# Kernel optimization log

Hardware: AMD Instinct MI355X
Metric: run time of the kernel (lower is better)

The kernel has to match this reference:

```python
import jax, jax.numpy as jnp
import numpy as np

N = 1024      # number of nodes
D = 128       # d_x
H = 8         # num_heads


def setup_inputs() -> dict:
    key = jax.random.key(0)
    ks = jax.random.split(key, 7)
    s = (D * H) ** -0.5
    return {
        "x": jax.random.normal(ks[0], (N, D), dtype=jnp.float32),
        "spatial_encoding": jax.random.normal(ks[1], (N, N), dtype=jnp.float32),
        "edge_encoding": jax.random.normal(ks[2], (N, N), dtype=jnp.float32),
        "Wq": jax.random.normal(ks[3], (D * H, D), dtype=jnp.float32) * s,
        "Wk": jax.random.normal(ks[4], (D * H, D), dtype=jnp.float32) * s,
        "Wv": jax.random.normal(ks[5], (D * H, D), dtype=jnp.float32) * s,
        "Wo": jax.random.normal(ks[6], (D, D * H), dtype=jnp.float32) * s,
    }


def reference(x, spatial_encoding, edge_encoding, Wq, Wk, Wv, Wo):
    n, d = x.shape
    h = Wq.shape[0] // d
    scale = d ** -0.5
    # Linear (no bias), then the module's peculiar view: [n, d*h] -> [d, n, h]
    q = (x @ Wq.T).reshape(d, n, h)            # [d, n, h]
    k = (x @ Wk.T).reshape(d, n, h)            # [d, n, h]
    v = (x @ Wv.T).reshape(d, n, h)            # [d, n, h]
    # a = q @ k^T over head dim: [d, n, n]
    a = jnp.einsum('dnh,dmh->dnm', q, k) * scale
    a = a + spatial_encoding + edge_encoding   # [n,n] biases broadcast over d
    a = jax.nn.softmax(a, axis=2)
    # dropout is identity at inference
    out = jnp.einsum('dnm,dmh->dnh', a, v)     # [d, n, h]
    out = out.reshape(n, h * d)                # row-major reshape, same as torch
    return out @ Wo.T                          # [n, d]
```

## Files before the change

### kernel.cpp

```cpp
#include <hip/hip_runtime.h>
#include <hip/hip_bf16.h>
#include <math.h>

#define N_NODES 1024
#define D_DIM   128
#define H_HEADS 8
#define DH      1024

typedef short  short8 __attribute__((ext_vector_type(8)));
typedef float  f32x16 __attribute__((ext_vector_type(16)));
typedef float  f32x4  __attribute__((ext_vector_type(4)));

static __device__ __forceinline__ unsigned short f2bf(float x) {
    __hip_bfloat16 h = __float2bfloat16(x);
    return *reinterpret_cast<unsigned short*>(&h);
}
static __device__ __forceinline__ unsigned cvt_pk_bf16(float lo, float hi) {
    unsigned r;
    asm volatile("v_cvt_pk_bf16_f32 %0, %1, %2" : "=v"(r) : "v"(lo), "v"(hi));
    return r;
}
static __device__ __forceinline__ void permlane32_swap(unsigned &a, unsigned &b) {
    asm volatile("v_permlane32_swap_b32 %0, %1" : "+v"(a), "+v"(b));
}
static __device__ __forceinline__ float fast_exp2(float x) {
    float r;
    asm("v_exp_f32 %0, %1" : "=v"(r) : "v"(x));
    return r;
}

__global__ __launch_bounds__(256) void prep_kernel(const float* __restrict__ x,
                                                   const float* __restrict__ Wq,
                                                   const float* __restrict__ Wk,
                                                   const float* __restrict__ Wv,
                                                   const float* __restrict__ sp,
                                                   const float* __restrict__ ed,
                                                   const float* __restrict__ Wo,
                                                   unsigned short* __restrict__ Q,
                                                   unsigned short* __restrict__ K,
                                                   unsigned short* __restrict__ V,
                                                   float* __restrict__ Bq,
                                                   unsigned short* __restrict__ Woh,
                                                   unsigned short* __restrict__ Wol) {
    __shared__ float tile[32][33];
    const int bid = blockIdx.x;
    const int tid = threadIdx.x;

    if (bid < 768) {
        const int lane = tid & 63, wvi = tid >> 6;
        const int l31 = lane & 31, hi = lane >> 5;
        const int m   = bid >> 8;
        const int rem = bid & 255;
        const int rb0 = (rem & 7) * 128 + wvi * 32;
        const int col = (rem >> 3) * 32 + l31;
        const float* W        = (m == 0) ? Wq : (m == 1) ? Wk : Wv;
        unsigned short* Out   = (m == 0) ? Q  : (m == 1) ? K  : V;
        const float osc = (m == 0) ? 0.12751879523173864f : 1.0f;

        const float* xrow = x + (size_t)(rb0 + l31) * 128 + 8 * hi;
        const float* wrow = W + (size_t)col * 128 + 8 * hi;

        f32x16 acc = {};
        #pragma unroll
        for (int ks = 0; ks < 8; ++ks) {
            float4 xa = *reinterpret_cast<const float4*>(xrow + ks * 16);
            float4 xb = *reinterpret_cast<const float4*>(xrow + ks * 16 + 4);
            float4 wa = *reinterpret_cast<const float4*>(wrow + ks * 16);
            float4 wb = *reinterpret_cast<const float4*>(wrow + ks * 16 + 4);
            union { short8 s8; unsigned u[4]; } af, bf;
            af.u[0] = cvt_pk_bf16(xa.x, xa.y); af.u[1] = cvt_pk_bf16(xa.z, xa.w);
            af.u[2] = cvt_pk_bf16(xb.x, xb.y); af.u[3] = cvt_pk_bf16(xb.z, xb.w);
            bf.u[0] = cvt_pk_bf16(wa.x, wa.y); bf.u[1] = cvt_pk_bf16(wa.z, wa.w);
            bf.u[2] = cvt_pk_bf16(wb.x, wb.y); bf.u[3] = cvt_pk_bf16(wb.z, wb.w);
            acc = __builtin_amdgcn_mfma_f32_32x32x16_bf16(af.s8, bf.s8, acc, 0, 0, 0);
        }
        #pragma unroll
        for (int i = 0; i < 16; ++i) {
            int mm = (i & 3) + 8 * (i >> 2) + 4 * hi;
            Out[(size_t)(rb0 + mm) * DH + col] = f2bf(acc[i] * osc);
        }
    } else if (bid < 1792) {
        const int b2 = bid - 768;
        const int cb = b2 & 31, rb = b2 >> 5;
        const float L2E = 1.4426950408889634f;
        for (int i = tid; i < 1024; i += 256) {
            int rr = i >> 5, cc = i & 31;
            size_t g = (size_t)(rb * 32 + rr) * 1024 + cb * 32 + cc;
            tile[rr][cc] = (sp[g] + ed[g]) * L2E;
        }
        __syncthreads();
        const int c4l = tid >> 5, rr = tid & 31;
        float4 v = make_float4(tile[rr][4 * c4l + 0], tile[rr][4 * c4l + 1],
                               tile[rr][4 * c4l + 2], tile[rr][4 * c4l + 3]);
        reinterpret_cast<float4*>(Bq)[(size_t)(cb * 8 + c4l) * 1024 + rb * 32 + rr] = v;
    } else {
        const int b2 = bid - 1792;
        const size_t base = (size_t)b2 * 4096 + (size_t)tid * 16;
        #pragma unroll
        for (int t = 0; t < 4; ++t) {
            float4 w = *reinterpret_cast<const float4*>(Wo + base + t * 4);
            float ww[4] = { w.x, w.y, w.z, w.w };
            unsigned short h4[4], l4[4];
            #pragma unroll
            for (int j = 0; j < 4; ++j) {
                unsigned uv = __float_as_uint(ww[j]);
                h4[j] = (unsigned short)(uv >> 16);
                l4[j] = f2bf(ww[j] - __uint_as_float(uv & 0xFFFF0000u));
            }
            *reinterpret_cast<uint2*>(Woh + base + t * 4) = *reinterpret_cast<uint2*>(h4);
            *reinterpret_cast<uint2*>(Wol + base + t * 4) = *reinterpret_cast<uint2*>(l4);
        }
    }
}

__global__ __launch_bounds__(256) void attn_kernel(const unsigned short* __restrict__ Qb,
                                                   const unsigned short* __restrict__ Kb,
                                                   const unsigned short* __restrict__ Vb,
                                                   const float* __restrict__ Bq,
                                                   float* __restrict__ Opart,
                                                   float* __restrict__ Lpart) {
    __shared__ unsigned short Vt[2][4608];
    const int dp = blockIdx.y, ch = blockIdx.z;
    const int tid = threadIdx.x, lane = tid & 63, wvi = tid >> 6;
    const int l31 = lane & 31, hi = lane >> 5;

    #pragma unroll
    for (int s = 0; s < 2; ++s) {
        const unsigned short* src = Vb + (size_t)(2 * dp + s) * 8192 + (size_t)ch * 4096;
        char* base = reinterpret_cast<char*>(&Vt[s][0]);
        int pr = tid;
        short8 v0 = *reinterpret_cast<const short8*>(src + (size_t)(2 * pr) * 8);
        short8 v1 = *reinterpret_cast<const short8*>(src + (size_t)(2 * pr + 1) * 8);
        #pragma unroll
        for (int h = 0; h < 8; ++h) {
            unsigned d = (unsigned)(unsigned short)v0[h] |
                         ((unsigned)(unsigned short)v1[h] << 16);
            *reinterpret_cast<unsigned*>(base + h * 1024 + ((4 * pr) ^ (h << 4))) = d;
        }
        reinterpret_cast<unsigned*>(base + 8 * 1024)[tid] = 0x3F803F80u;
    }
    __syncthreads();

    const int r = blockIdx.x * 128 + wvi * 32 + l31;
    short8 qf0 = {}, qf1 = {};
    if (!hi) {
        qf0 = *reinterpret_cast<const short8*>(Qb + (size_t)(2 * dp)     * 8192 + (size_t)r * 8);
        qf1 = *reinterpret_cast<const short8*>(Qb + (size_t)(2 * dp + 1) * 8192 + (size_t)r * 8);
    }

    f32x16 o0 = {}, o1 = {};
    const unsigned short* kp0 = Kb + (size_t)(2 * dp) * 8192 + (size_t)(ch * 512 + l31) * 8;
    const unsigned short* kp1 = kp0 + 8192;
    const float4* bq4 = reinterpret_cast<const float4*>(Bq)
                        + (size_t)ch * 131072 + (size_t)hi * 1024 + r;
    const int vrow = (l31 < 8) ? l31 : 8;
    const char* vb0 = reinterpret_cast<const char*>(&Vt[0][0]) + vrow * 1024;
    const char* vb1 = reinterpret_cast<const char*>(&Vt[1][0]) + vrow * 1024;
    const int vswz = vrow << 4;

    auto load_bias = [&](int cbv) -> f32x16 {
        const float4* b = bq4 + (size_t)cbv * 8192;
        float4 b0 = b[0], b1 = b[2048], b2 = b[4096], b3 = b[6144];
        f32x16 o;
        o[0]  = b0.x; o[1]  = b0.y; o[2]  = b0.z; o[3]  = b0.w;
        o[4]  = b1.x; o[5]  = b1.y; o[6]  = b1.z; o[7]  = b1.w;
        o[8]  = b2.x; o[9]  = b2.y; o[10] = b2.z; o[11] = b2.w;
        o[12] = b3.x; o[13] = b3.y; o[14] = b3.z; o[15] = b3.w;
        return o;
    };
    auto slice_step = [&](int cbv, const f32x16& bias, const short8& kfv,
                          const short8& qfv, const char* vbs, f32x16& oaccs) {
        f32x16 sf = bias;
        sf = __builtin_amdgcn_mfma_f32_32x32x16_bf16(kfv, qfv, sf, 0, 0, 0);
        float p[16];
        #pragma unroll
        for (int i = 0; i < 16; ++i) p[i] = fast_exp2(sf[i]);
        unsigned u0 = cvt_pk_bf16(p[0],  p[1]);
        unsigned u1 = cvt_pk_bf16(p[2],  p[3]);
        unsigned u2 = cvt_pk_bf16(p[4],  p[5]);
        unsigned u3 = cvt_pk_bf16(p[6],  p[7]);
        unsigned u4 = cvt_pk_bf16(p[8],  p[9]);
        unsigned u5 = cvt_pk_bf16(p[10], p[11]);
        unsigned u6 = cvt_pk_bf16(p[12], p[13]);
        unsigned u7 = cvt_pk_bf16(p[14], p[15]);
        permlane32_swap(u0, u2);
        permlane32_swap(u1, u3);
        permlane32_swap(u4, u6);
        permlane32_swap(u5, u7);
        union { short8 s8; unsigned u[4]; } pb1, pb2;
        pb1.u[0] = u0; pb1.u[1] = u1; pb1.u[2] = u2; pb1.u[3] = u3;
        pb2.u[0] = u4; pb2.u[1] = u5; pb2.u[2] = u6; pb2.u[3] = u7;

        short8 vf1 = *reinterpret_cast<const short8*>(vbs + ((cbv * 64 + 16 * hi)      ^ vswz));
        short8 vf2 = *reinterpret_cast<const short8*>(vbs + ((cbv * 64 + 32 + 16 * hi) ^ vswz));
        oaccs = __builtin_amdgcn_mfma_f32_32x32x16_bf16(vf1, pb1.s8, oaccs, 0, 0, 0);
        oaccs = __builtin_amdgcn_mfma_f32_32x32x16_bf16(vf2, pb2.s8, oaccs, 0, 0, 0);
    };
    auto load_k = [&](const unsigned short* kp, int cbv) -> short8 {
        return *reinterpret_cast<const short8*>(kp + (size_t)cbv * 256);
    };

    f32x16 bA = load_bias(0), bB = load_bias(1);
    short8 kA0 = load_k(kp0, 0), kA1 = load_k(kp1, 0);
    short8 kB0 = load_k(kp0, 1), kB1 = load_k(kp1, 1);
    for (int cb = 0; cb < 16; cb += 2) {
        slice_step(cb, bA, kA0, qf0, vb0, o0);
        slice_step(cb, bA, kA1, qf1, vb1, o1);
        if (cb < 14) { bA = load_bias(cb + 2); kA0 = load_k(kp0, cb + 2); kA1 = load_k(kp1, cb + 2); }
        slice_step(cb + 1, bB, kB0, qf0, vb0, o0);
        slice_step(cb + 1, bB, kB1, qf1, vb1, o1);
        if (cb < 14) { bB = load_bias(cb + 3); kB0 = load_k(kp0, cb + 3); kB1 = load_k(kp1, cb + 3); }
    }

    #pragma unroll
    for (int s = 0; s < 2; ++s) {
        const f32x16& oa = s ? o1 : o0;
        const int dd = 2 * dp + s;
        size_t off = (size_t)ch * 1048576 + (size_t)dd * 8192 + (size_t)r * 8 + 4 * hi;
        *reinterpret_cast<float4*>(Opart + off) =
            make_float4(oa[0], oa[1], oa[2], oa[3]);
        if (!hi) Lpart[(size_t)ch * 131072 + (size_t)dd * 1024 + r] = oa[4];
    }
}

__global__ __launch_bounds__(256) void combine_kernel(const float* __restrict__ Opart,
                                                      const float* __restrict__ Lpart,
                                                      unsigned short* __restrict__ Oh,
                                                      unsigned short* __restrict__ Ol) {
    const int gid = blockIdx.x * 256 + threadIdx.x;
    const float4* p1 = reinterpret_cast<const float4*>(Opart) + (size_t)gid * 2;
    const float4* p2 = reinterpret_cast<const float4*>(Opart + 1048576) + (size_t)gid * 2;
    float4 a0 = p1[0], a1 = p1[1], b0 = p2[0], b1 = p2[1];
    const float rl = 1.f / (Lpart[gid] + Lpart[131072 + gid]);
    float v[8] = { (a0.x + b0.x) * rl, (a0.y + b0.y) * rl,
                   (a0.z + b0.z) * rl, (a0.w + b0.w) * rl,
                   (a1.x + b1.x) * rl, (a1.y + b1.y) * rl,
                   (a1.z + b1.z) * rl, (a1.w + b1.w) * rl };
    union { short8 s8; unsigned short us[8]; } h8, l8;
    #pragma unroll
    for (int i = 0; i < 8; ++i) {
        unsigned uv = __float_as_uint(v[i]);
        h8.us[i] = (unsigned short)(uv >> 16);
        l8.us[i] = f2bf(v[i] - __uint_as_float(uv & 0xFFFF0000u));
    }
    *reinterpret_cast<short8*>(Oh + (size_t)gid * 8) = h8.s8;
    *reinterpret_cast<short8*>(Ol + (size_t)gid * 8) = l8.s8;
}

__global__ __launch_bounds__(256) void oproj_kernel(const unsigned short* __restrict__ Oh,
                                                    const unsigned short* __restrict__ Ol,
                                                    const unsigned short* __restrict__ Woh,
                                                    const unsigned short* __restrict__ Wol,
                                                    float* __restrict__ out) {
    __shared__ float red[4][256];
    const int tid = threadIdx.x, lane = tid & 63, wvi = tid >> 6;
    const int l15 = lane & 15, kg = lane >> 4;
    const int rbase = blockIdx.x * 16, cbase = blockIdx.y * 16;

    const unsigned short* ah_p = Oh  + (size_t)(rbase + l15) * 1024 + wvi * 256 + kg * 8;
    const unsigned short* al_p = Ol  + (size_t)(rbase + l15) * 1024 + wvi * 256 + kg * 8;
    const unsigned short* bh_p = Woh + (size_t)(cbase + l15) * 1024 + wvi * 256 + kg * 8;
    const unsigned short* bl_p = Wol + (size_t)(cbase + l15) * 1024 + wvi * 256 + kg * 8;

    f32x4 acc = {};
    #pragma unroll
    for (int ks = 0; ks < 8; ++ks) {
        short8 ah = *reinterpret_cast<const short8*>(ah_p + ks * 32);
        short8 al = *reinterpret_cast<const short8*>(al_p + ks * 32);
        short8 bh = *reinterpret_cast<const short8*>(bh_p + ks * 32);
        short8 bl = *reinterpret_cast<const short8*>(bl_p + ks * 32);
        acc = __builtin_amdgcn_mfma_f32_16x16x32_bf16(ah, bh, acc, 0, 0, 0);
        acc = __builtin_amdgcn_mfma_f32_16x16x32_bf16(al, bh, acc, 0, 0, 0);
        acc = __builtin_amdgcn_mfma_f32_16x16x32_bf16(ah, bl, acc, 0, 0, 0);
    }
    #pragma unroll
    for (int i = 0; i < 4; ++i)
        red[wvi][(kg * 4 + i) * 16 + l15] = acc[i];
    __syncthreads();
    float v = red[0][tid & 255] + red[1][tid & 255] + red[2][tid & 255] + red[3][tid & 255];
    out[(size_t)(rbase + (tid >> 4)) * D_DIM + cbase + (tid & 15)] = v;
}

extern "C" void kernel_launch(void* const* d_in, const int* in_sizes, int n_in,
                              void* d_out, int out_size, void* d_ws, size_t ws_size,
                              hipStream_t stream) {
    const float* x  = (const float*)d_in[0];
    const float* sp = (const float*)d_in[1];
    const float* ed = (const float*)d_in[2];
    const float* Wq = (const float*)d_in[3];
    const float* Wk = (const float*)d_in[4];
    const float* Wv = (const float*)d_in[5];
    const float* Wo = (const float*)d_in[6];
    float* out = (float*)d_out;

    float* ws = (float*)d_ws;
    const size_t M = (size_t)N_NODES * DH;
    float* Bq = ws;
    unsigned short* Qb = (unsigned short*)(ws + M);
    unsigned short* Kb = Qb + M;
    unsigned short* Vb = Kb + M;
    unsigned short* Oh = Vb + M;
    unsigned short* Ol = Oh + M;
    float* Opart = (float*)(Ol + M);
    float* Lpart = Opart + 2 * M;
    unsigned short* Woh = (unsigned short*)(Lpart + 2 * 131072);
    unsigned short* Wol = Woh + 131072;

    prep_kernel<<<dim3(1824), 256, 0, stream>>>(x, Wq, Wk, Wv, sp, ed, Wo,
                                                Qb, Kb, Vb, Bq, Woh, Wol);
    attn_kernel<<<dim3(8, 64, 2), 256, 0, stream>>>(Qb, Kb, Vb, Bq, Opart, Lpart);
    combine_kernel<<<dim3(512), 256, 0, stream>>>(Opart, Lpart, Oh, Ol);
    oproj_kernel<<<dim3(64, 8), 256, 0, stream>>>(Oh, Ol, Woh, Wol, out);
}
```

Baseline: 62.97 us.

## Drop split-key attention and combine kernel; process all keys per block

The attention kernel no longer splits the 1024 keys into two chunks across blocks. Each block now stages all of V into LDS (doubled footprint) and loops over 32 key tiles, then normalizes and writes hi/lo bf16 outputs directly. This removes the combine kernel launch and the fp32 partial-output round trip through global memory. The cost is half as many blocks for the attention phase, with longer per-block loops and more LDS per block, which may lower occupancy.

```diff
diff --git a/kernel.cpp b/kernel.cpp
--- a/kernel.cpp
+++ b/kernel.cpp
@@ -29,32 +29,27 @@
     return r;
 }
 
-__global__ __launch_bounds__(256) void prep_kernel(const float* __restrict__ x,
-                                                   const float* __restrict__ Wq,
-                                                   const float* __restrict__ Wk,
-                                                   const float* __restrict__ Wv,
-                                                   const float* __restrict__ sp,
-                                                   const float* __restrict__ ed,
-                                                   const float* __restrict__ Wo,
-                                                   unsigned short* __restrict__ Q,
-                                                   unsigned short* __restrict__ K,
-                                                   unsigned short* __restrict__ V,
-                                                   float* __restrict__ Bq,
-                                                   unsigned short* __restrict__ Woh,
-                                                   unsigned short* __restrict__ Wol) {
+__global__ __launch_bounds__(256) void prep_kernel(
+        const float* __restrict__ x,  const float* __restrict__ Wq,
+        const float* __restrict__ Wk, const float* __restrict__ Wv,
+        const float* __restrict__ sp, const float* __restrict__ ed,
+        const float* __restrict__ Wo,
+        unsigned short* __restrict__ Qb, unsigned short* __restrict__ Kb,
+        unsigned short* __restrict__ Vb, float* __restrict__ Bq,
+        unsigned short* __restrict__ Woh, unsigned short* __restrict__ Wol) {
     __shared__ float tile[32][33];
-    const int bid = blockIdx.x;
+    const int u   = blockIdx.x;
     const int tid = threadIdx.x;
 
-    if (bid < 768) {
+    if (u < 768) {
         const int lane = tid & 63, wvi = tid >> 6;
         const int l31 = lane & 31, hi = lane >> 5;
-        const int m   = bid >> 8;
-        const int rem = bid & 255;
+        const int m   = u >> 8;
+        const int rem = u & 255;
         const int rb0 = (rem & 7) * 128 + wvi * 32;
         const int col = (rem >> 3) * 32 + l31;
         const float* W        = (m == 0) ? Wq : (m == 1) ? Wk : Wv;
-        unsigned short* Out   = (m == 0) ? Q  : (m == 1) ? K  : V;
+        unsigned short* Out   = (m == 0) ? Qb : (m == 1) ? Kb : Vb;
         const float osc = (m == 0) ? 0.12751879523173864f : 1.0f;
 
         const float* xrow = x + (size_t)(rb0 + l31) * 128 + 8 * hi;
@@ -67,11 +62,11 @@
             float4 xb = *reinterpret_cast<const float4*>(xrow + ks * 16 + 4);
             float4 wa = *reinterpret_cast<const float4*>(wrow + ks * 16);
             float4 wb = *reinterpret_cast<const float4*>(wrow + ks * 16 + 4);
-            union { short8 s8; unsigned u[4]; } af, bf;
-            af.u[0] = cvt_pk_bf16(xa.x, xa.y); af.u[1] = cvt_pk_bf16(xa.z, xa.w);
-            af.u[2] = cvt_pk_bf16(xb.x, xb.y); af.u[3] = cvt_pk_bf16(xb.z, xb.w);
-            bf.u[0] = cvt_pk_bf16(wa.x, wa.y); bf.u[1] = cvt_pk_bf16(wa.z, wa.w);
-            bf.u[2] = cvt_pk_bf16(wb.x, wb.y); bf.u[3] = cvt_pk_bf16(wb.z, wb.w);
+            union { short8 s8; unsigned uu[4]; } af, bf;
+            af.uu[0] = cvt_pk_bf16(xa.x, xa.y); af.uu[1] = cvt_pk_bf16(xa.z, xa.w);
+            af.uu[2] = cvt_pk_bf16(xb.x, xb.y); af.uu[3] = cvt_pk_bf16(xb.z, xb.w);
+            bf.uu[0] = cvt_pk_bf16(wa.x, wa.y); bf.uu[1] = cvt_pk_bf16(wa.z, wa.w);
+            bf.uu[2] = cvt_pk_bf16(wb.x, wb.y); bf.uu[3] = cvt_pk_bf16(wb.z, wb.w);
             acc = __builtin_amdgcn_mfma_f32_32x32x16_bf16(af.s8, bf.s8, acc, 0, 0, 0);
         }
         #pragma unroll
@@ -79,8 +74,8 @@
             int mm = (i & 3) + 8 * (i >> 2) + 4 * hi;
             Out[(size_t)(rb0 + mm) * DH + col] = f2bf(acc[i] * osc);
         }
-    } else if (bid < 1792) {
-        const int b2 = bid - 768;
+    } else if (u < 1792) {
+        const int b2 = u - 768;
         const int cb = b2 & 31, rb = b2 >> 5;
         const float L2E = 1.4426950408889634f;
         for (int i = tid; i < 1024; i += 256) {
@@ -94,7 +89,7 @@
                                tile[rr][4 * c4l + 2], tile[rr][4 * c4l + 3]);
         reinterpret_cast<float4*>(Bq)[(size_t)(cb * 8 + c4l) * 1024 + rb * 32 + rr] = v;
     } else {
-        const int b2 = bid - 1792;
+        const int b2 = u - 1792;
         const size_t base = (size_t)b2 * 4096 + (size_t)tid * 16;
         #pragma unroll
         for (int t = 0; t < 4; ++t) {
@@ -113,149 +108,147 @@
     }
 }
 
-__global__ __launch_bounds__(256) void attn_kernel(const unsigned short* __restrict__ Qb,
-                                                   const unsigned short* __restrict__ Kb,
-                                                   const unsigned short* __restrict__ Vb,
-                                                   const float* __restrict__ Bq,
-                                                   float* __restrict__ Opart,
-                                                   float* __restrict__ Lpart) {
-    __shared__ unsigned short Vt[2][4608];
-    const int dp = blockIdx.y, ch = blockIdx.z;
-    const int tid = threadIdx.x, lane = tid & 63, wvi = tid >> 6;
-    const int l31 = lane & 31, hi = lane >> 5;
-
-    #pragma unroll
-    for (int s = 0; s < 2; ++s) {
-        const unsigned short* src = Vb + (size_t)(2 * dp + s) * 8192 + (size_t)ch * 4096;
-        char* base = reinterpret_cast<char*>(&Vt[s][0]);
-        int pr = tid;
+static __device__ __forceinline__ void stage_vt(const unsigned short* __restrict__ src,
+                                                char* base, int tid) {
+    #pragma unroll
+    for (int it = 0; it < 2; ++it) {
+        int pr = it * 256 + tid;
         short8 v0 = *reinterpret_cast<const short8*>(src + (size_t)(2 * pr) * 8);
         short8 v1 = *reinterpret_cast<const short8*>(src + (size_t)(2 * pr + 1) * 8);
         #pragma unroll
         for (int h = 0; h < 8; ++h) {
             unsigned d = (unsigned)(unsigned short)v0[h] |
                          ((unsigned)(unsigned short)v1[h] << 16);
-            *reinterpret_cast<unsigned*>(base + h * 1024 + ((4 * pr) ^ (h << 4))) = d;
-        }
-        reinterpret_cast<unsigned*>(base + 8 * 1024)[tid] = 0x3F803F80u;
-    }
+            *reinterpret_cast<unsigned*>(base + h * 2048 + ((4 * pr) ^ (h << 4))) = d;
+        }
+    }
+    reinterpret_cast<unsigned*>(base + 16384)[tid]       = 0x3F803F80u;
+    reinterpret_cast<unsigned*>(base + 16384)[tid + 256] = 0x3F803F80u;
+}
+
+static __device__ __forceinline__ f32x16 load_bias16(const float4* bq4, int cbv) {
+    const float4* b = bq4 + (size_t)cbv * 8192;
+    float4 b0 = b[0], b1 = b[2048], b2 = b[4096], b3 = b[6144];
+    f32x16 o;
+    o[0]  = b0.x; o[1]  = b0.y; o[2]  = b0.z; o[3]  = b0.w;
+    o[4]  = b1.x; o[5]  = b1.y; o[6]  = b1.z; o[7]  = b1.w;
+    o[8]  = b2.x; o[9]  = b2.y; o[10] = b2.z; o[11] = b2.w;
+    o[12] = b3.x; o[13] = b3.y; o[14] = b3.z; o[15] = b3.w;
+    return o;
+}
+
+static __device__ __forceinline__ void attn_step(int cbv, const f32x16& bias,
+                                                 const short8& kfv, const short8& qfv,
+                                                 const char* vbs, int vswz, int hi,
+                                                 f32x16& oacc) {
+    f32x16 sf = bias;
+    sf = __builtin_amdgcn_mfma_f32_32x32x16_bf16(kfv, qfv, sf, 0, 0, 0);
+    float p[16];
+    #pragma unroll
+    for (int i = 0; i < 16; ++i) p[i] = fast_exp2(sf[i]);
+    unsigned u0 = cvt_pk_bf16(p[0],  p[1]);
+    unsigned u1 = cvt_pk_bf16(p[2],  p[3]);
+    unsigned u2 = cvt_pk_bf16(p[4],  p[5]);
+    unsigned u3 = cvt_pk_bf16(p[6],  p[7]);
+    unsigned u4 = cvt_pk_bf16(p[8],  p[9]);
+    unsigned u5 = cvt_pk_bf16(p[10], p[11]);
+    unsigned u6 = cvt_pk_bf16(p[12], p[13]);
+    unsigned u7 = cvt_pk_bf16(p[14], p[15]);
+    permlane32_swap(u0, u2);
+    permlane32_swap(u1, u3);
+    permlane32_swap(u4, u6);
+    permlane32_swap(u5, u7);
+    union { short8 s8; unsigned uu[4]; } pb1, pb2;
+    pb1.uu[0] = u0; pb1.uu[1] = u1; pb1.uu[2] = u2; pb1.uu[3] = u3;
+    pb2.uu[0] = u4; pb2.uu[1] = u5; pb2.uu[2] = u6; pb2.uu[3] = u7;
+
+    short8 vf1 = *reinterpret_cast<const short8*>(vbs + ((cbv * 64 + 16 * hi)      ^ vswz));
+    short8 vf2 = *reinterpret_cast<const short8*>(vbs + ((cbv * 64 + 32 + 16 * hi) ^ vswz));
+    oacc = __builtin_amdgcn_mfma_f32_32x32x16_bf16(vf1, pb1.s8, oacc, 0, 0, 0);
+    oacc = __builtin_amdgcn_mfma_f32_32x32x16_bf16(vf2, pb2.s8, oacc, 0, 0, 0);
+}
+
+static __device__ __forceinline__ void attn_epilogue(const f32x16& oa, int dd, int r, int hi,
+                                                     unsigned short* __restrict__ Oh,
+                                                     unsigned short* __restrict__ Ol) {
+    const float ls = oa[4];
+    const float rl = 1.f / ls;
+    unsigned short h4[4], l4[4];
+    #pragma unroll
+    for (int i = 0; i < 4; ++i) {
+        float v = oa[i] * rl;
+        unsigned uv = __float_as_uint(v);
+        h4[i] = (unsigned short)(uv >> 16);
+        l4[i] = f2bf(v - __uint_as_float(uv & 0xFFFF0000u));
+    }
+    size_t off = (size_t)dd * 8192 + (size_t)r * 8 + 4 * hi;
+    *reinterpret_cast<uint2*>(Oh + off) = *reinterpret_cast<uint2*>(h4);
+    *reinterpret_cast<uint2*>(Ol + off) = *reinterpret_cast<uint2*>(l4);
+}
+
+__global__ __launch_bounds__(256) void attn2_kernel(
+        const unsigned short* __restrict__ Qb, const unsigned short* __restrict__ Kb,
+        const unsigned short* __restrict__ Vb, const float* __restrict__ Bq,
+        unsigned short* __restrict__ Oh, unsigned short* __restrict__ Ol) {
+    __shared__ __align__(16) char smraw[36864];
+    const int un = blockIdx.x, tid = threadIdx.x;
+    const int rbx = un & 7, dp = un >> 3;
+    const int lane = tid & 63, wvi = tid >> 6;
+    const int l31 = lane & 31, hi = lane >> 5;
+
+    stage_vt(Vb + (size_t)(2 * dp) * 8192,     smraw,         tid);
+    stage_vt(Vb + (size_t)(2 * dp + 1) * 8192, smraw + 18432, tid);
     __syncthreads();
 
-    const int r = blockIdx.x * 128 + wvi * 32 + l31;
+    const int r = rbx * 128 + wvi * 32 + l31;
     short8 qf0 = {}, qf1 = {};
     if (!hi) {
         qf0 = *reinterpret_cast<const short8*>(Qb + (size_t)(2 * dp)     * 8192 + (size_t)r * 8);
         qf1 = *reinterpret_cast<const short8*>(Qb + (size_t)(2 * dp + 1) * 8192 + (size_t)r * 8);
     }
-
     f32x16 o0 = {}, o1 = {};
-    const unsigned short* kp0 = Kb + (size_t)(2 * dp) * 8192 + (size_t)(ch * 512 + l31) * 8;
+    const unsigned short* kp0 = Kb + (size_t)(2 * dp) * 8192 + (size_t)l31 * 8;
     const unsigned short* kp1 = kp0 + 8192;
-    const float4* bq4 = reinterpret_cast<const float4*>(Bq)
-                        + (size_t)ch * 131072 + (size_t)hi * 1024 + r;
+    const float4* bq4 = reinterpret_cast<const float4*>(Bq) + (size_t)hi * 1024 + r;
     const int vrow = (l31 < 8) ? l31 : 8;
-    const char* vb0 = reinterpret_cast<const char*>(&Vt[0][0]) + vrow * 1024;
-    const char* vb1 = reinterpret_cast<const char*>(&Vt[1][0]) + vrow * 1024;
+    const char* vb0 = smraw + vrow * 2048;
+    const char* vb1 = smraw + 18432 + vrow * 2048;
     const int vswz = vrow << 4;
 
-    auto load_bias = [&](int cbv) -> f32x16 {
-        const float4* b = bq4 + (size_t)cbv * 8192;
-        float4 b0 = b[0], b1 = b[2048], b2 = b[4096], b3 = b[6144];
-        f32x16 o;
-        o[0]  = b0.x; o[1]  = b0.y; o[2]  = b0.z; o[3]  = b0.w;
-        o[4]  = b1.x; o[5]  = b1.y; o[6]  = b1.z; o[7]  = b1.w;
-        o[8]  = b2.x; o[9]  = b2.y; o[10] = b2.z; o[11] = b2.w;
-        o[12] = b3.x; o[13] = b3.y; o[14] = b3.z; o[15] = b3.w;
-        return o;
-    };
-    auto slice_step = [&](int cbv, const f32x16& bias, const short8& kfv,
-                          const short8& qfv, const char* vbs, f32x16& oaccs) {
-        f32x16 sf = bias;
-        sf = __builtin_amdgcn_mfma_f32_32x32x16_bf16(kfv, qfv, sf, 0, 0, 0);
-        float p[16];
-        #pragma unroll
-        for (int i = 0; i < 16; ++i) p[i] = fast_exp2(sf[i]);
-        unsigned u0 = cvt_pk_bf16(p[0],  p[1]);
-        unsigned u1 = cvt_pk_bf16(p[2],  p[3]);
-        unsigned u2 = cvt_pk_bf16(p[4],  p[5]);
-        unsigned u3 = cvt_pk_bf16(p[6],  p[7]);
-        unsigned u4 = cvt_pk_bf16(p[8],  p[9]);
-        unsigned u5 = cvt_pk_bf16(p[10], p[11]);
-        unsigned u6 = cvt_pk_bf16(p[12], p[13]);
-        unsigned u7 = cvt_pk_bf16(p[14], p[15]);
-        permlane32_swap(u0, u2);
-        permlane32_swap(u1, u3);
-        permlane32_swap(u4, u6);
-        permlane32_swap(u5, u7);
-        union { short8 s8; unsigned u[4]; } pb1, pb2;
-        pb1.u[0] = u0; pb1.u[1] = u1; pb1.u[2] = u2; pb1.u[3] = u3;
-        pb2.u[0] = u4; pb2.u[1] = u5; pb2.u[2] = u6; pb2.u[3] = u7;
-
-        short8 vf1 = *reinterpret_cast<const short8*>(vbs + ((cbv * 64 + 16 * hi)      ^ vswz));
-        short8 vf2 = *reinterpret_cast<const short8*>(vbs + ((cbv * 64 + 32 + 16 * hi) ^ vswz));
-        oaccs = __builtin_amdgcn_mfma_f32_32x32x16_bf16(vf1, pb1.s8, oaccs, 0, 0, 0);
-        oaccs = __builtin_amdgcn_mfma_f32_32x32x16_bf16(vf2, pb2.s8, oaccs, 0, 0, 0);
-    };
-    auto load_k = [&](const unsigned short* kp, int cbv) -> short8 {
-        return *reinterpret_cast<const short8*>(kp + (size_t)cbv * 256);
-    };
-
-    f32x16 bA = load_bias(0), bB = load_bias(1);
-    short8 kA0 = load_k(kp0, 0), kA1 = load_k(kp1, 0);
-    short8 kB0 = load_k(kp0, 1), kB1 = load_k(kp1, 1);
-    for (int cb = 0; cb < 16; cb += 2) {
-        slice_step(cb, bA, kA0, qf0, vb0, o0);
-        slice_step(cb, bA, kA1, qf1, vb1, o1);
-        if (cb < 14) { bA = load_bias(cb + 2); kA0 = load_k(kp0, cb + 2); kA1 = load_k(kp1, cb + 2); }
-        slice_step(cb + 1, bB, kB0, qf0, vb0, o0);
-        slice_step(cb + 1, bB, kB1, qf1, vb1, o1);
-        if (cb < 14) { bB = load_bias(cb + 3); kB0 = load_k(kp0, cb + 3); kB1 = load_k(kp1, cb + 3); }
-    }
-
-    #pragma unroll
-    for (int s = 0; s < 2; ++s) {
-        const f32x16& oa = s ? o1 : o0;
-        const int dd = 2 * dp + s;
-        size_t off = (size_t)ch * 1048576 + (size_t)dd * 8192 + (size_t)r * 8 + 4 * hi;
-        *reinterpret_cast<float4*>(Opart + off) =
-            make_float4(oa[0], oa[1], oa[2], oa[3]);
-        if (!hi) Lpart[(size_t)ch * 131072 + (size_t)dd * 1024 + r] = oa[4];
-    }
-}
-
-__global__ __launch_bounds__(256) void combine_kernel(const float* __restrict__ Opart,
-                                                      const float* __restrict__ Lpart,
-                                                      unsigned short* __restrict__ Oh,
-                                                      unsigned short* __restrict__ Ol) {
-    const int gid = blockIdx.x * 256 + threadIdx.x;
-    const float4* p1 = reinterpret_cast<const float4*>(Opart) + (size_t)gid * 2;
-    const float4* p2 = reinterpret_cast<const float4*>(Opart + 1048576) + (size_t)gid * 2;
-    float4 a0 = p1[0], a1 = p1[1], b0 = p2[0], b1 = p2[1];
-    const float rl = 1.f / (Lpart[gid] + Lpart[131072 + gid]);
-    float v[8] = { (a0.x + b0.x) * rl, (a0.y + b0.y) * rl,
-                   (a0.z + b0.z) * rl, (a0.w + b0.w) * rl,
-                   (a1.x + b1.x) * rl, (a1.y + b1.y) * rl,
-                   (a1.z + b1.z) * rl, (a1.w + b1.w) * rl };
-    union { short8 s8; unsigned short us[8]; } h8, l8;
-    #pragma unroll
-    for (int i = 0; i < 8; ++i) {
-        unsigned uv = __float_as_uint(v[i]);
-        h8.us[i] = (unsigned short)(uv >> 16);
-        l8.us[i] = f2bf(v[i] - __uint_as_float(uv & 0xFFFF0000u));
-    }
-    *reinterpret_cast<short8*>(Oh + (size_t)gid * 8) = h8.s8;
-    *reinterpret_cast<short8*>(Ol + (size_t)gid * 8) = l8.s8;
-}
-
-__global__ __launch_bounds__(256) void oproj_kernel(const unsigned short* __restrict__ Oh,
-                                                    const unsigned short* __restrict__ Ol,
-                                                    const unsigned short* __restrict__ Woh,
-                                                    const unsigned short* __restrict__ Wol,
-                                                    float* __restrict__ out) {
+    f32x16 bA = load_bias16(bq4, 0), bB = load_bias16(bq4, 1);
+    short8 kA0 = *reinterpret_cast<const short8*>(kp0);
+    short8 kA1 = *reinterpret_cast<const short8*>(kp1);
+    short8 kB0 = *reinterpret_cast<const short8*>(kp0 + 256);
+    short8 kB1 = *reinterpret_cast<const short8*>(kp1 + 256);
+    for (int cb = 0; cb < 32; cb += 2) {
+        attn_step(cb, bA, kA0, qf0, vb0, vswz, hi, o0);
+        attn_step(cb, bA, kA1, qf1, vb1, vswz, hi, o1);
+        if (cb < 30) {
+            bA = load_bias16(bq4, cb + 2);
+            kA0 = *reinterpret_cast<const short8*>(kp0 + (size_t)(cb + 2) * 256);
+            kA1 = *reinterpret_cast<const short8*>(kp1 + (size_t)(cb + 2) * 256);
+        }
+        attn_step(cb + 1, bB, kB0, qf0, vb0, vswz, hi, o0);
+        attn_step(cb + 1, bB, kB1, qf1, vb1, vswz, hi, o1);
+        if (cb < 30) {
+            bB = load_bias16(bq4, cb + 3);
+            kB0 = *reinterpret_cast<const short8*>(kp0 + (size_t)(cb + 3) * 256);
+            kB1 = *reinterpret_cast<const short8*>(kp1 + (size_t)(cb + 3) * 256);
+        }
+    }
+    attn_epilogue(o0, 2 * dp,     r, hi, Oh, Ol);
+    attn_epilogue(o1, 2 * dp + 1, r, hi, Oh, Ol);
+}
+
+__global__ __launch_bounds__(256) void oproj_kernel(
+        const unsigned short* __restrict__ Oh, const unsigned short* __restrict__ Ol,
+        const unsigned short* __restrict__ Woh, const unsigned short* __restrict__ Wol,
+        float* __restrict__ out) {
     __shared__ float red[4][256];
-    const int tid = threadIdx.x, lane = tid & 63, wvi = tid >> 6;
+    const int u = blockIdx.x, tid = threadIdx.x;
+    const int lane = tid & 63, wvi = tid >> 6;
     const int l15 = lane & 15, kg = lane >> 4;
-    const int rbase = blockIdx.x * 16, cbase = blockIdx.y * 16;
+    const int rbase = (u & 63) * 16, cbase = (u >> 6) * 16;
 
     const unsigned short* ah_p = Oh  + (size_t)(rbase + l15) * 1024 + wvi * 256 + kg * 8;
     const unsigned short* al_p = Ol  + (size_t)(rbase + l15) * 1024 + wvi * 256 + kg * 8;
@@ -301,14 +294,11 @@
     unsigned short* Vb = Kb + M;
     unsigned short* Oh = Vb + M;
     unsigned short* Ol = Oh + M;
-    float* Opart = (float*)(Ol + M);
-    float* Lpart = Opart + 2 * M;
-    unsigned short* Woh = (unsigned short*)(Lpart + 2 * 131072);
+    unsigned short* Woh = Ol + M;
     unsigned short* Wol = Woh + 131072;
 
     prep_kernel<<<dim3(1824), 256, 0, stream>>>(x, Wq, Wk, Wv, sp, ed, Wo,
                                                 Qb, Kb, Vb, Bq, Woh, Wol);
-    attn_kernel<<<dim3(8, 64, 2), 256, 0, stream>>>(Qb, Kb, Vb, Bq, Opart, Lpart);
-    combine_kernel<<<dim3(512), 256, 0, stream>>>(Opart, Lpart, Oh, Ol);
-    oproj_kernel<<<dim3(64, 8), 256, 0, stream>>>(Oh, Ol, Woh, Wol, out);
-}
+    attn2_kernel<<<dim3(512), 256, 0, stream>>>(Qb, Kb, Vb, Bq, Oh, Ol);
+    oproj_kernel<<<dim3(512), 256, 0, stream>>>(Oh, Ol, Woh, Wol, out);
+}
```

After: 61.18 us (median of 2 runs). 1.03x faster.
